# Kernel optimization log

Hardware: AMD Instinct MI355X
Metric: run time of the kernel (lower is better)

The kernel has to match this reference:

```python
import jax, jax.numpy as jnp
import numpy as np

LOG_STD_MAX = 2.0
LOG_STD_MIN = -5.0
N_EXPERTS = 16
TOPK = 4
OBS = 512
ACT = 256
BATCH = 16384


def setup_inputs() -> dict:
    key = jax.random.key(0)
    ks = jax.random.split(key, 7)
    s_obs = 1.0 / np.sqrt(OBS)
    return {
        "x": jax.random.normal(ks[0], (BATCH, OBS), dtype=jnp.float32),
        "router_w": jax.random.uniform(ks[1], (N_EXPERTS, OBS), jnp.float32, -s_obs, s_obs),
        "router_b": jax.random.uniform(ks[2], (N_EXPERTS,), jnp.float32, -s_obs, s_obs),
        "mean_w": jax.random.uniform(ks[3], (N_EXPERTS, ACT, OBS), jnp.float32, -s_obs, s_obs),
        "mean_b": jax.random.uniform(ks[4], (N_EXPERTS, ACT), jnp.float32, -s_obs, s_obs),
        "log_std_w": jax.random.uniform(ks[5], (N_EXPERTS, ACT, OBS), jnp.float32, -s_obs, s_obs),
        "log_std_b": jax.random.uniform(ks[6], (N_EXPERTS, ACT), jnp.float32, -s_obs, s_obs),
        "router_noise": 0,
    }


def reference(x, router_w, router_b, mean_w, mean_b, log_std_w, log_std_b, router_noise):
    # router_noise=0 -> deterministic path (training-time noise omitted)
    B = x.shape[0]
    router_logits = x @ router_w.T + router_b                    # [B, E]
    router_probs = jax.nn.softmax(router_logits, axis=-1)         # [B, E]
    topk_probs, topk_idx = jax.lax.top_k(router_probs, TOPK)      # [B, K]
    sparse_probs = jnp.zeros_like(router_probs).at[
        jnp.arange(B)[:, None], topk_idx
    ].set(topk_probs)                                             # [B, E]

    # all-expert dense stack: [B, E, A]
    expert_out = jnp.einsum("bo,eao->bea", x, mean_w) + mean_b
    log_std_out = jnp.einsum("bo,eao->bea", x, log_std_w) + log_std_b

    w = sparse_probs[:, :, None]                                  # [B, E, 1]
    mean = jnp.sum(expert_out * w, axis=1)                        # [B, A]
    log_std = jnp.sum(log_std_out * w, axis=1)                    # [B, A]
    log_std = jnp.tanh(log_std)
    log_std = LOG_STD_MIN + 0.5 * (LOG_STD_MAX - LOG_STD_MIN) * (log_std + 1.0)
    return mean, log_std
```

## Files before the change

kernel.cpp:

```cpp
#include <hip/hip_runtime.h>
#include <math.h>

#define BB   16384
#define OBS  512
#define NE   16
#define ACTD 256
#define TK   4

#define WS_ROWLIST_OFF  ((size_t)64)
#define WS_PROBLIST_OFF (WS_ROWLIST_OFF + (size_t)NE * BB * 4)
#define WS_SLOT_OFF     (WS_PROBLIST_OFF + (size_t)NE * BB * 4)
#define WS_XBF_OFF      (WS_SLOT_OFF + (size_t)NE * BB * 4)
#define WS_WM_OFF       (WS_XBF_OFF + (size_t)BB * OBS * 2)
#define WS_WL_OFF       (WS_WM_OFF + (size_t)NE * ACTD * OBS * 2)
#define WS_PART_OFF     (WS_WL_OFF + (size_t)NE * ACTD * OBS * 2)
#define WS_NEEDED_A2    (WS_PART_OFF + (size_t)2 * BB * TK * ACTD * 2)

typedef __attribute__((ext_vector_type(8))) short short8;
typedef __attribute__((ext_vector_type(4))) float floatx4;

__device__ __forceinline__ ushort f2bf(float f) {
    union { float f; unsigned u; } v; v.f = f;
    unsigned r = v.u + 0x7fffu + ((v.u >> 16) & 1u);
    return (ushort)(r >> 16);
}
__device__ __forceinline__ float bf2f(ushort u) {
    union { unsigned u; float f; } v; v.u = ((unsigned)u) << 16;
    return v.f;
}
__device__ __forceinline__ float lstd_act(float v) {
    return -5.f + 7.f * __builtin_amdgcn_rcpf(1.f + __expf(-2.f * v));
}

__global__ __launch_bounds__(256) void router_kernel(
    const float* __restrict__ x, const float* __restrict__ rw,
    const float* __restrict__ rb,
    int* __restrict__ counts, int* __restrict__ rowlist,
    float* __restrict__ problist, int* __restrict__ slot_of,
    ushort* __restrict__ xbf,
    const float* __restrict__ mwf, const float* __restrict__ lwf,
    ushort* __restrict__ wmbf, ushort* __restrict__ wlbf, int do_aux)
{
    __shared__ float wlds[NE * OBS];
    __shared__ int   lcnt[NE], lbase[NE];
    __shared__ int   s_e[64], s_lpos[64];
    __shared__ float s_p[64];

    const float4* rw4 = (const float4*)rw;
    float4* wl4 = (float4*)wlds;
    #pragma unroll
    for (int i = 0; i < 8; ++i) wl4[threadIdx.x + 256 * i] = rw4[threadIdx.x + 256 * i];
    if (threadIdx.x < NE) lcnt[threadIdx.x] = 0;
    __syncthreads();

    const int wave = threadIdx.x >> 6;
    const int lane = threadIdx.x & 63;
    const int q    = lane >> 4;
    const int i16  = lane & 15;
    const int row  = blockIdx.x * 16 + wave * 4 + q;

    const float4* xr = (const float4*)(x + (size_t)row * OBS);
    float4 xv[8];
    #pragma unroll
    for (int s = 0; s < 8; ++s) xv[s] = xr[s * 16 + i16];

    if (do_aux) {
        ushort4* xo = (ushort4*)(xbf + (size_t)row * OBS);
        #pragma unroll
        for (int s = 0; s < 8; ++s) {
            ushort4 o;
            o.x = f2bf(xv[s].x); o.y = f2bf(xv[s].y);
            o.z = f2bf(xv[s].z); o.w = f2bf(xv[s].w);
            xo[s * 16 + i16] = o;
        }
    }

    float p[NE];
    float m = -1e30f;
    #pragma unroll
    for (int e = 0; e < NE; ++e) {
        const float4* wep = (const float4*)(wlds + e * OBS);
        float d = 0.f;
        #pragma unroll
        for (int s = 0; s < 8; ++s) {
            float4 wv = wep[s * 16 + i16];
            d += xv[s].x * wv.x + xv[s].y * wv.y + xv[s].z * wv.z + xv[s].w * wv.w;
        }
        d += __shfl_xor(d, 1, 64);
        d += __shfl_xor(d, 2, 64);
        d += __shfl_xor(d, 4, 64);
        d += __shfl_xor(d, 8, 64);
        d += rb[e];
        p[e] = d;
        m = fmaxf(m, d);
    }
    float s = 0.f;
    #pragma unroll
    for (int e = 0; e < NE; ++e) { p[e] = __expf(p[e] - m); s += p[e]; }
    const float inv = 1.f / s;
    #pragma unroll
    for (int e = 0; e < NE; ++e) p[e] *= inv;

    int   sel_e[TK];
    float sel_p[TK];
    #pragma unroll
    for (int k = 0; k < TK; ++k) {
        float best = -1.f; int be = 0;
        #pragma unroll
        for (int e = 0; e < NE; ++e)
            if (p[e] > best) { best = p[e]; be = e; }
        sel_e[k] = be; sel_p[k] = best;
        #pragma unroll
        for (int e = 0; e < NE; ++e)
            if (e == be) p[e] = -2.f;
    }
    if (i16 < TK) {
        const int e = sel_e[i16];
        const int lpos = atomicAdd(&lcnt[e], 1);
        const int sid = (wave * 4 + q) * 4 + i16;
        s_e[sid] = e; s_p[sid] = sel_p[i16]; s_lpos[sid] = lpos;
    }
    __syncthreads();
    if (threadIdx.x < NE)
        lbase[threadIdx.x] = atomicAdd(&counts[threadIdx.x], lcnt[threadIdx.x]);
    __syncthreads();
    if (threadIdx.x < 64) {
        const int sid = threadIdx.x;
        const int e   = s_e[sid];
        const int pos = lbase[e] + s_lpos[sid];
        const int grow = blockIdx.x * 16 + (sid >> 2);
        rowlist[e * BB + pos]  = grow;
        problist[e * BB + pos] = s_p[sid];
        if (do_aux) slot_of[e * BB + pos] = grow * TK + (sid & 3);
    }

    if (do_aux) {
        const int gid = blockIdx.x * 256 + threadIdx.x;
        const float4* m4 = (const float4*)mwf;
        const float4* l4 = (const float4*)lwf;
        ushort4* mo = (ushort4*)wmbf;
        ushort4* lo = (ushort4*)wlbf;
        #pragma unroll
        for (int j = 0; j < 2; ++j) {
            const int idx = gid + 262144 * j;
            float4 a = m4[idx];
            ushort4 oa;
            oa.x = f2bf(a.x); oa.y = f2bf(a.y); oa.z = f2bf(a.z); oa.w = f2bf(a.w);
            mo[idx] = oa;
            float4 b = l4[idx];
            ushort4 ob;
            ob.x = f2bf(b.x); ob.y = f2bf(b.y); ob.z = f2bf(b.z); ob.w = f2bf(b.w);
            lo[idx] = ob;
        }
    }
}

__global__ __launch_bounds__(256, 4) void moe_gemm_128(
    const ushort* __restrict__ xbf,
    const ushort* __restrict__ wmean, const ushort* __restrict__ wlstd,
    const float* __restrict__ mean_b, const float* __restrict__ lstd_b,
    const int* __restrict__ counts, const int* __restrict__ rowlist,
    const float* __restrict__ problist, const int* __restrict__ slot_of,
    ushort* __restrict__ partial)
{
    const int flat = blockIdx.x + 528 * blockIdx.y;
    const int virt = (flat & 7) * 264 + (flat >> 3);
    const int zz   = virt & 3;
    const int gt   = virt >> 2;

    int e = -1, tile0 = 0, cnt = 0, tsum = 0;
    #pragma unroll
    for (int ee = 0; ee < NE; ++ee) {
        const int ce = counts[ee];
        const int nt = (ce + 127) >> 7;
        if (e < 0 && gt < tsum + nt) { e = ee; tile0 = (gt - tsum) * 128; cnt = ce; }
        tsum += nt;
    }
    if (e < 0) return;

    const int which = zz >> 1;
    const int ctile = (zz & 1) * 128;
    const ushort* W   = (which ? wlstd : wmean) + (size_t)e * ACTD * OBS;
    const float* bias = (which ? lstd_b : mean_b) + e * ACTD + ctile;
    ushort* Pp = partial + (size_t)which * BB * TK * ACTD;

    __shared__ __align__(16) ushort xls[128 * 64];
    __shared__ __align__(16) ushort wls[128 * 64];

    const int tid = threadIdx.x;
    const int l   = tid & 63;
    const int w   = tid >> 6;

    const int c_sw = (l & 7) ^ (l >> 3);
    const ushort* xp[4];
    #pragma unroll
    for (int i = 0; i < 4; ++i) {
        const int lrow = 32 * w + 8 * i + (l >> 3);
        const int pos  = tile0 + lrow;
        const int grow = (pos < cnt) ? rowlist[e * BB + pos] : rowlist[e * BB + tile0];
        xp[i] = xbf + (size_t)grow * OBS + c_sw * 8;
    }
    const ushort* wp[4];
    #pragma unroll
    for (int j = 0; j < 4; ++j) {
        const int col = ctile + 32 * w + 8 * j + (l >> 3);
        wp[j] = W + (size_t)col * OBS + c_sw * 8;
    }

    const int wm  = (w >> 1) * 64;
    const int wn  = (w & 1) * 64;
    const int rlo = l & 15;
    const int q   = l >> 4;
    const int r7  = rlo & 7;

    floatx4 acc[4][4];
    #pragma unroll
    for (int mi = 0; mi < 4; ++mi)
        #pragma unroll
        for (int ni = 0; ni < 4; ++ni)
            acc[mi][ni] = (floatx4){0.f, 0.f, 0.f, 0.f};

    for (int kt = 0; kt < OBS; kt += 64) {
        __syncthreads();
        #pragma unroll
        for (int i = 0; i < 4; ++i)
            __builtin_amdgcn_global_load_lds(
                (const __attribute__((address_space(1))) unsigned int*)(xp[i] + kt),
                (__attribute__((address_space(3))) unsigned int*)(xls + (4 * w + i) * 512),
                16, 0, 0);
        #pragma unroll
        for (int j = 0; j < 4; ++j)
            __builtin_amdgcn_global_load_lds(
                (const __attribute__((address_space(1))) unsigned int*)(wp[j] + kt),
                (__attribute__((address_space(3))) unsigned int*)(wls + (4 * w + j) * 512),
                16, 0, 0);
        __syncthreads();

        #pragma unroll
        for (int ks = 0; ks < 2; ++ks) {
            const int ch = (4 * ks + q) ^ r7;
            short8 af[4], bfr[4];
            #pragma unroll
            for (int mi = 0; mi < 4; ++mi)
                af[mi] = *(const short8*)(xls + (wm + mi * 16 + rlo) * 64 + ch * 8);
            #pragma unroll
            for (int ni = 0; ni < 4; ++ni)
                bfr[ni] = *(const short8*)(wls + (wn + ni * 16 + rlo) * 64 + ch * 8);
            #pragma unroll
            for (int mi = 0; mi < 4; ++mi)
                #pragma unroll
                for (int ni = 0; ni < 4; ++ni)
                    acc[mi][ni] = __builtin_amdgcn_mfma_f32_16x16x32_bf16(
                        af[mi], bfr[ni], acc[mi][ni], 0, 0, 0);
        }
    }

    #pragma unroll
    for (int mi = 0; mi < 4; ++mi) {
        #pragma unroll
        for (int r = 0; r < 4; ++r) {
            const int lrow = wm + mi * 16 + q * 4 + r;
            const int pos  = tile0 + lrow;
            if (pos >= cnt) continue;
            const int slot = slot_of[e * BB + pos];
            const float pw = problist[e * BB + pos];
            ushort* orow = Pp + (size_t)slot * ACTD + ctile + wn + rlo;
            #pragma unroll
            for (int ni = 0; ni < 4; ++ni)
                orow[ni * 16] = f2bf(pw * (acc[mi][ni][r] + bias[wn + ni * 16 + rlo]));
        }
    }
}

__global__ __launch_bounds__(256) void combine_kernel(
    const ushort* __restrict__ partial, float* __restrict__ out)
{
    const int t  = blockIdx.x * 256 + threadIdx.x;
    const int r  = t >> 5;
    const int c8 = (t & 31) * 8;
    const ushort* Pm = partial;
    const ushort* Pl = partial + (size_t)BB * TK * ACTD;

    float sm[8] = {}, sl[8] = {};
    #pragma unroll
    for (int k = 0; k < TK; ++k) {
        const size_t off = (size_t)(r * TK + k) * ACTD + c8;
        short8 vm = *(const short8*)(Pm + off);
        short8 vl = *(const short8*)(Pl + off);
        #pragma unroll
        for (int j = 0; j < 8; ++j) {
            sm[j] += bf2f((ushort)vm[j]);
            sl[j] += bf2f((ushort)vl[j]);
        }
    }
    float4 mo0 = make_float4(sm[0], sm[1], sm[2], sm[3]);
    float4 mo1 = make_float4(sm[4], sm[5], sm[6], sm[7]);
    float4 lo0 = make_float4(lstd_act(sl[0]), lstd_act(sl[1]), lstd_act(sl[2]), lstd_act(sl[3]));
    float4 lo1 = make_float4(lstd_act(sl[4]), lstd_act(sl[5]), lstd_act(sl[6]), lstd_act(sl[7]));
    float* om = out + (size_t)r * ACTD + c8;
    float* ol = out + (size_t)BB * ACTD + (size_t)r * ACTD + c8;
    *(float4*)(om)     = mo0;
    *(float4*)(om + 4) = mo1;
    *(float4*)(ol)     = lo0;
    *(float4*)(ol + 4) = lo1;
}

__global__ __launch_bounds__(256) void moe_gemm_f32(
    const float* __restrict__ x,
    const float* __restrict__ mean_w, const float* __restrict__ mean_b,
    const float* __restrict__ lstd_w, const float* __restrict__ lstd_b,
    const int* __restrict__ counts, const int* __restrict__ rowlist,
    const float* __restrict__ problist, float* __restrict__ out)
{
    const int e = blockIdx.y;
    const int cnt = counts[e];
    const int tile0 = blockIdx.x * 32;
    if (tile0 >= cnt) return;

    const int zz    = blockIdx.z;
    const int which = zz >> 1;
    const int ctile = (zz & 1) * 128;
    const float* W    = (which ? lstd_w : mean_w) + (size_t)e * ACTD * OBS;
    const float* bias = (which ? lstd_b : mean_b) + e * ACTD;
    float* outp = out + (size_t)which * BB * ACTD;

    __shared__ float xls[32][32];
    __shared__ float wls[32][128];

    const int sr  = threadIdx.x >> 3;
    const int skq = threadIdx.x & 7;
    int stage_row = -1;
    {
        const int pos = tile0 + sr;
        if (pos < cnt) stage_row = rowlist[e * BB + pos];
    }

    const int r0 = (threadIdx.x >> 5) << 2;
    const int c0 = (threadIdx.x & 31) << 2;

    float acc[4][4] = {};

    for (int kt = 0; kt < OBS; kt += 32) {
        __syncthreads();
        {
            float4 v = make_float4(0.f, 0.f, 0.f, 0.f);
            if (stage_row >= 0)
                v = *(const float4*)(x + (size_t)stage_row * OBS + kt + skq * 4);
            xls[skq * 4 + 0][sr] = v.x;
            xls[skq * 4 + 1][sr] = v.y;
            xls[skq * 4 + 2][sr] = v.z;
            xls[skq * 4 + 3][sr] = v.w;
        }
        #pragma unroll
        for (int j = 0; j < 4; ++j) {
            const int i  = threadIdx.x + 256 * j;
            const int c  = i >> 3;
            const int kq = i & 7;
            float4 v = *(const float4*)(W + (size_t)(ctile + c) * OBS + kt + kq * 4);
            wls[kq * 4 + 0][c] = v.x;
            wls[kq * 4 + 1][c] = v.y;
            wls[kq * 4 + 2][c] = v.z;
            wls[kq * 4 + 3][c] = v.w;
        }
        __syncthreads();

        #pragma unroll
        for (int k = 0; k < 32; ++k) {
            const float4 xa = *(const float4*)&xls[k][r0];
            const float4 wb = *(const float4*)&wls[k][c0];
            const float xv[4] = { xa.x, xa.y, xa.z, xa.w };
            const float wv[4] = { wb.x, wb.y, wb.z, wb.w };
            #pragma unroll
            for (int i = 0; i < 4; ++i)
                #pragma unroll
                for (int j = 0; j < 4; ++j)
                    acc[i][j] = fmaf(xv[i], wv[j], acc[i][j]);
        }
    }

    #pragma unroll
    for (int i = 0; i < 4; ++i) {
        const int pos = tile0 + r0 + i;
        if (pos >= cnt) break;
        const int grow = rowlist[e * BB + pos];
        const float pw = problist[e * BB + pos];
        float* orow = outp + (size_t)grow * ACTD + ctile + c0;
        #pragma unroll
        for (int j = 0; j < 4; ++j)
            atomicAdd(&orow[j], pw * (acc[i][j] + bias[ctile + c0 + j]));
    }
}

__global__ __launch_bounds__(256) void tanh_ep(float* __restrict__ out)
{
    const int i = blockIdx.x * 256 + threadIdx.x;
    float4* p = (float4*)(out + (size_t)BB * ACTD);
    float4 v = p[i];
    v.x = -5.f + 3.5f * (tanhf(v.x) + 1.f);
    v.y = -5.f + 3.5f * (tanhf(v.y) + 1.f);
    v.z = -5.f + 3.5f * (tanhf(v.z) + 1.f);
    v.w = -5.f + 3.5f * (tanhf(v.w) + 1.f);
    p[i] = v;
}

extern "C" void kernel_launch(void* const* d_in, const int* in_sizes, int n_in,
                              void* d_out, int out_size, void* d_ws, size_t ws_size,
                              hipStream_t stream)
{
    const float* x        = (const float*)d_in[0];
    const float* router_w = (const float*)d_in[1];
    const float* router_b = (const float*)d_in[2];
    const float* mean_w   = (const float*)d_in[3];
    const float* mean_b   = (const float*)d_in[4];
    const float* lstd_w   = (const float*)d_in[5];
    const float* lstd_b   = (const float*)d_in[6];

    float* out = (float*)d_out;
    int*    counts   = (int*)d_ws;
    int*    rowlist  = (int*)((char*)d_ws + WS_ROWLIST_OFF);
    float*  problist = (float*)((char*)d_ws + WS_PROBLIST_OFF);
    int*    slot_of  = (int*)((char*)d_ws + WS_SLOT_OFF);
    ushort* xbf      = (ushort*)((char*)d_ws + WS_XBF_OFF);
    ushort* wmbf     = (ushort*)((char*)d_ws + WS_WM_OFF);
    ushort* wlbf     = (ushort*)((char*)d_ws + WS_WL_OFF);
    ushort* partial  = (ushort*)((char*)d_ws + WS_PART_OFF);

    const bool tierA2 = (ws_size >= WS_NEEDED_A2);

    if (tierA2) {
        hipMemsetAsync(d_ws, 0, 64, stream);

        router_kernel<<<BB / 16, 256, 0, stream>>>(x, router_w, router_b,
                                                   counts, rowlist, problist,
                                                   slot_of, xbf,
                                                   mean_w, lstd_w, wmbf, wlbf, 1);

        dim3 grid(528, 4);
        moe_gemm_128<<<grid, 256, 0, stream>>>(xbf, wmbf, wlbf, mean_b, lstd_b,
                                               counts, rowlist, problist,
                                               slot_of, partial);
        combine_kernel<<<BB * 32 / 256, 256, 0, stream>>>(partial, out);
    } else {
        hipMemsetAsync(d_ws, 0, 64, stream);
        hipMemsetAsync(d_out, 0, (size_t)out_size * sizeof(float), stream);
        router_kernel<<<BB / 16, 256, 0, stream>>>(x, router_w, router_b,
                                                   counts, rowlist, problist,
                                                   (int*)nullptr, (ushort*)nullptr,
                                                   (const float*)nullptr,
                                                   (const float*)nullptr,
                                                   (ushort*)nullptr, (ushort*)nullptr, 0);
        dim3 grid(BB / 32, NE, 4);
        moe_gemm_f32<<<grid, 256, 0, stream>>>(x, mean_w, mean_b, lstd_w, lstd_b,
                                               counts, rowlist, problist, out);
        tanh_ep<<<(BB * ACTD / 4) / 256, 256, 0, stream>>>(out);
    }
}
```

Before: 192.0 us.

## Double-buffer LDS tiles in MoE GEMM to overlap global loads with MFMA

Splits the shared-memory X and W tiles into two buffers so the next K-step's global-to-LDS loads are issued before the current step's MFMAs run. It replaces __syncthreads with explicit vmcnt/lgkmcnt waits and s_barrier, and fully unrolls the K loop. The aim is to hide global memory latency behind compute. In exchange LDS per block doubles to 64KB and the occupancy hint drops from 4 to 2 blocks per CU, which may cut latency hiding across blocks.

```diff
diff --git a/kernel.cpp b/kernel.cpp
--- a/kernel.cpp
+++ b/kernel.cpp
@@ -155,7 +155,7 @@
     }
 }
 
-__global__ __launch_bounds__(256, 4) void moe_gemm_128(
+__global__ __launch_bounds__(256, 2) void moe_gemm_128(
     const ushort* __restrict__ xbf,
     const ushort* __restrict__ wmean, const ushort* __restrict__ wlstd,
     const float* __restrict__ mean_b, const float* __restrict__ lstd_b,
@@ -184,8 +184,8 @@
     const float* bias = (which ? lstd_b : mean_b) + e * ACTD + ctile;
     ushort* Pp = partial + (size_t)which * BB * TK * ACTD;
 
-    __shared__ __align__(16) ushort xls[128 * 64];
-    __shared__ __align__(16) ushort wls[128 * 64];
+    __shared__ __align__(16) ushort xls[2][128 * 64];
+    __shared__ __align__(16) ushort wls[2][128 * 64];
 
     const int tid = threadIdx.x;
     const int l   = tid & 63;
@@ -220,21 +220,35 @@
         for (int ni = 0; ni < 4; ++ni)
             acc[mi][ni] = (floatx4){0.f, 0.f, 0.f, 0.f};
 
-    for (int kt = 0; kt < OBS; kt += 64) {
-        __syncthreads();
-        #pragma unroll
-        for (int i = 0; i < 4; ++i)
-            __builtin_amdgcn_global_load_lds(
-                (const __attribute__((address_space(1))) unsigned int*)(xp[i] + kt),
-                (__attribute__((address_space(3))) unsigned int*)(xls + (4 * w + i) * 512),
-                16, 0, 0);
-        #pragma unroll
-        for (int j = 0; j < 4; ++j)
-            __builtin_amdgcn_global_load_lds(
-                (const __attribute__((address_space(1))) unsigned int*)(wp[j] + kt),
-                (__attribute__((address_space(3))) unsigned int*)(wls + (4 * w + j) * 512),
-                16, 0, 0);
-        __syncthreads();
+#define STAGE(B, KT)                                                          \
+    do {                                                                      \
+        _Pragma("unroll")                                                     \
+        for (int i = 0; i < 4; ++i)                                           \
+            __builtin_amdgcn_global_load_lds(                                 \
+                (const __attribute__((address_space(1))) unsigned int*)(xp[i] + (KT)), \
+                (__attribute__((address_space(3))) unsigned int*)(&xls[B][(4 * w + i) * 512]), \
+                16, 0, 0);                                                    \
+        _Pragma("unroll")                                                     \
+        for (int j = 0; j < 4; ++j)                                           \
+            __builtin_amdgcn_global_load_lds(                                 \
+                (const __attribute__((address_space(1))) unsigned int*)(wp[j] + (KT)), \
+                (__attribute__((address_space(3))) unsigned int*)(&wls[B][(4 * w + j) * 512]), \
+                16, 0, 0);                                                    \
+    } while (0)
+
+    STAGE(0, 0);
+
+    #pragma unroll
+    for (int kt_i = 0; kt_i < 8; ++kt_i) {
+        const int b = kt_i & 1;
+        if (kt_i < 7) {
+            STAGE(b ^ 1, (kt_i + 1) * 64);
+            asm volatile("s_waitcnt vmcnt(8)" ::: "memory");
+        } else {
+            asm volatile("s_waitcnt vmcnt(0)" ::: "memory");
+        }
+        __builtin_amdgcn_s_barrier();
+        __builtin_amdgcn_sched_barrier(0);
 
         #pragma unroll
         for (int ks = 0; ks < 2; ++ks) {
@@ -242,10 +256,10 @@
             short8 af[4], bfr[4];
             #pragma unroll
             for (int mi = 0; mi < 4; ++mi)
-                af[mi] = *(const short8*)(xls + (wm + mi * 16 + rlo) * 64 + ch * 8);
+                af[mi] = *(const short8*)(&xls[b][(wm + mi * 16 + rlo) * 64 + ch * 8]);
             #pragma unroll
             for (int ni = 0; ni < 4; ++ni)
-                bfr[ni] = *(const short8*)(wls + (wn + ni * 16 + rlo) * 64 + ch * 8);
+                bfr[ni] = *(const short8*)(&wls[b][(wn + ni * 16 + rlo) * 64 + ch * 8]);
             #pragma unroll
             for (int mi = 0; mi < 4; ++mi)
                 #pragma unroll
@@ -253,7 +267,12 @@
                     acc[mi][ni] = __builtin_amdgcn_mfma_f32_16x16x32_bf16(
                         af[mi], bfr[ni], acc[mi][ni], 0, 0, 0);
         }
-    }
+        __builtin_amdgcn_sched_barrier(0);
+        asm volatile("s_waitcnt lgkmcnt(0)" ::: "memory");
+        __builtin_amdgcn_s_barrier();
+        __builtin_amdgcn_sched_barrier(0);
+    }
+#undef STAGE
 
     #pragma unroll
     for (int mi = 0; mi < 4; ++mi) {
```

Result: slower. 208.4 us (+8.5%).
